# Optimization experiments

Measured on AMD Instinct MI355X. Metric: run time of the kernel, lower is better.

## Reference

```python
import jax, jax.numpy as jnp
import numpy as np

B, S, D, H, W = 4, 2048, 512, 8, 16
DK = D // H


def setup_inputs() -> dict:
    key = jax.random.key(0)
    ks = jax.random.split(key, 11)
    scale = 1.0 / np.sqrt(D)
    return {
        "query": jax.random.normal(ks[0], (B, S, D), jnp.float32),
        "key": jax.random.normal(ks[1], (B, S, D), jnp.float32),
        "value": jax.random.normal(ks[2], (B, S, D), jnp.float32),
        "Wq": jax.random.normal(ks[3], (D, D), jnp.float32) * scale,
        "bq": jnp.zeros((D,), jnp.float32),
        "Wk": jax.random.normal(ks[4], (D, D), jnp.float32) * scale,
        "bk": jnp.zeros((D,), jnp.float32),
        "Wv": jax.random.normal(ks[5], (D, D), jnp.float32) * scale,
        "bv": jnp.zeros((D,), jnp.float32),
        "Wo": jax.random.normal(ks[6], (D, D), jnp.float32) * scale,
        "bo": jnp.zeros((D,), jnp.float32),
    }


def reference(query, key, value, Wq, bq, Wk, bk, Wv, bv, Wo, bo):
    b, s, d = query.shape
    # QKV projections -> [b, H, s, DK]
    Q = (query @ Wq + bq).reshape(b, s, H, DK).transpose(0, 2, 1, 3)
    K = (key @ Wk + bk).reshape(b, s, H, DK).transpose(0, 2, 1, 3)
    V = (value @ Wv + bv).reshape(b, s, H, DK).transpose(0, 2, 1, 3)
    # Dense scores (faithful to original O(n^2) math), then static band mask
    scores = jnp.einsum("bhqd,bhkd->bhqk", Q, K) / jnp.sqrt(jnp.array(DK, scores_dtype := Q.dtype))
    idx = jnp.arange(s)
    local = jnp.abs(idx[:, None] - idx[None, :]) <= W  # [s, s] band
    mask_value = jnp.finfo(scores.dtype).min
    scores = jnp.where(local[None, None], scores, mask_value)
    attn = jax.nn.softmax(scores, axis=-1)
    ctx = jnp.einsum("bhqk,bhkd->bhqd", attn, V)
    ctx = ctx.transpose(0, 2, 1, 3).reshape(b, s, d)
    return ctx @ Wo + bo
```

## Files before the change

### kernel.cpp

```cpp
#include <hip/hip_runtime.h>

typedef __attribute__((ext_vector_type(8))) short bf16x8;
typedef __attribute__((ext_vector_type(4))) float f32x4;
typedef __attribute__((ext_vector_type(4))) unsigned int u32x4;
typedef __attribute__((ext_vector_type(8))) unsigned short bfu8;
typedef __attribute__((ext_vector_type(4))) unsigned short bfu4;

#define BB 4
#define SS 2048
#define DD 512
#define HH 8
#define DKK 64
#define WWIN 16
#define MTOT (BB*SS)
#define MKE  ((long)MTOT*DD)
#define NKE  ((long)DD*DD)

__device__ __forceinline__ unsigned short f2bf(float f) {
  unsigned int u = __float_as_uint(f);
  u += 0x7fffu + ((u >> 16) & 1u);
  return (unsigned short)(u >> 16);
}
__device__ __forceinline__ float bf2f(unsigned short s) {
  return __uint_as_float(((unsigned int)s) << 16);
}

__device__ __forceinline__ void gload_lds16(const unsigned short* g, unsigned short* l) {
  __builtin_amdgcn_global_load_lds((const __attribute__((address_space(1))) void*)g,
                                   (__attribute__((address_space(3))) void*)l, 16, 0, 0);
}

__global__ __launch_bounds__(256) void convert_w(
    const float* __restrict__ Wq, const float* __restrict__ Wk,
    const float* __restrict__ Wv, const float* __restrict__ Wo,
    const float* __restrict__ bq, const float* __restrict__ bk, const float* __restrict__ bv,
    unsigned short* __restrict__ wt, float* __restrict__ bias_all)
{
  int bx = blockIdx.x;
  if (bx >= 256) {
    int idx = (bx - 256) * 256 + threadIdx.x;
    bias_all[idx] = idx < DD ? bq[idx] : (idx < 2*DD ? bk[idx-DD] : bv[idx-2*DD]);
    return;
  }
  int wm = bx >> 6;
  int tile = bx & 63;
  int tr = tile >> 3, tc = tile & 7;
  const float* src = wm==0 ? Wq : wm==1 ? Wk : wm==2 ? Wv : Wo;
  unsigned short* dst = wt + (long)wm*NKE;
  __shared__ float tl[64][65];
  int t = threadIdx.x;
  int cr = t >> 6;
  int cc = t & 63;
  for (int p = 0; p < 16; ++p) {
    int row = p*4 + cr;
    tl[row][cc] = src[(long)(tr*64+row)*DD + tc*64 + cc];
  }
  __syncthreads();
  for (int p = 0; p < 16; ++p) {
    int orow = p*4 + cr;
    dst[(long)(tc*64 + orow)*DD + tr*64 + cc] = f2bf(tl[cc][orow]);
  }
}

template<int OUT_BF16, int A_FP32>
__global__ __launch_bounds__(256, 2) void gemm_kernel(
    const void* __restrict__ a0, const void* __restrict__ a1, const void* __restrict__ a2,
    const unsigned short* __restrict__ Btbase, long bZ,
    const float* __restrict__ biasBase, long biasZ,
    void* __restrict__ outBase, long outZ,
    int M, int N, int K)
{
  const int z = blockIdx.z;
  const void* Av = z==0 ? a0 : z==1 ? a1 : a2;
  const unsigned short* Bt = Btbase + (long)z*bZ;
  const float* bias = biasBase + (long)z*biasZ;

  const int tid  = threadIdx.x;
  const int lane = tid & 63;
  const int w    = tid >> 6;
  const int wr   = w >> 1, wc = w & 1;
  const int m0   = blockIdx.y * 128;
  const int n0   = blockIdx.x * 128;

  __shared__ unsigned short lA[128*64];
  __shared__ unsigned short lB[128*64];

  f32x4 acc[4][4] = {};

  for (int kt = 0; kt < K; kt += 64) {
    for (int i = 0; i < 4; ++i) {
      int e   = (w*4+i)*512 + lane*8;
      int row = e >> 6, col = e & 63;
      gload_lds16(Bt + (long)(n0 + row)*K + kt + col, &lB[(w*4+i)*512]);
    }
    if (A_FP32) {
      const float* Afp = (const float*)Av;
      for (int i = 0; i < 8; ++i) {
        int e   = (i*256 + tid) * 4;
        int row = e >> 6, col = e & 63;
        float4 f = *(const float4*)(Afp + (long)(m0 + row)*K + kt + col);
        bfu4 o;
        o[0]=f2bf(f.x); o[1]=f2bf(f.y); o[2]=f2bf(f.z); o[3]=f2bf(f.w);
        *(bfu4*)(&lA[e]) = o;
      }
    } else {
      const unsigned short* A = (const unsigned short*)Av;
      for (int i = 0; i < 4; ++i) {
        int e   = (w*4+i)*512 + lane*8;
        int row = e >> 6, col = e & 63;
        gload_lds16(A + (long)(m0 + row)*K + kt + col, &lA[(w*4+i)*512]);
      }
    }
    __syncthreads();
    for (int kk = 0; kk < 2; ++kk) {
      bf16x8 af[4], bfr[4];
      for (int m = 0; m < 4; ++m) {
        int row = wr*64 + m*16 + (lane & 15);
        af[m] = *reinterpret_cast<const bf16x8*>(&lA[row*64 + kk*32 + (lane>>4)*8]);
      }
      for (int n = 0; n < 4; ++n) {
        int col = wc*64 + n*16 + (lane & 15);
        bfr[n] = *reinterpret_cast<const bf16x8*>(&lB[col*64 + kk*32 + (lane>>4)*8]);
      }
      for (int m = 0; m < 4; ++m)
        for (int n = 0; n < 4; ++n)
          acc[m][n] = __builtin_amdgcn_mfma_f32_16x16x32_bf16(af[m], bfr[n], acc[m][n], 0, 0, 0);
    }
    __syncthreads();
  }

  for (int m = 0; m < 4; ++m) {
    int rbase = m0 + wr*64 + m*16 + ((lane>>4)<<2);
    for (int n = 0; n < 4; ++n) {
      int col = n0 + wc*64 + n*16 + (lane & 15);
      float bv = bias[col];
      for (int r = 0; r < 4; ++r) {
        float val = acc[m][n][r] + bv;
        long idx = (long)z*outZ + (long)(rbase + r)*N + col;
        if (OUT_BF16) ((unsigned short*)outBase)[idx] = f2bf(val);
        else          ((float*)outBase)[idx] = val;
      }
    }
  }
}

#define KP 76
#define PP 76
__global__ __launch_bounds__(256) void attn_kernel(
    const unsigned short* __restrict__ Qbf, const unsigned short* __restrict__ Kbf,
    const unsigned short* __restrict__ Vbf, unsigned short* __restrict__ ctxbf)
{
  const int q0 = blockIdx.x * 128;
  const int h  = blockIdx.y;
  const int b  = blockIdx.z;
  const int tid = threadIdx.x, lane = tid & 63, w = tid >> 6;
  const int c = lane & 15, g = lane >> 4;
  const int w0 = q0 - WWIN;

  __shared__ unsigned short K_l[160*KP];
  __shared__ unsigned short V_l[160*KP];
  __shared__ unsigned short P_l[4][32*PP];

  const long baseRow = (long)b*SS*DD + (long)h*DKK;
  const int qw0   = q0 + w*32;
  const int kbase = w*32;

  bf16x8 aq[2][2];
  for (int m = 0; m < 2; ++m)
    for (int kk = 0; kk < 2; ++kk)
      aq[m][kk] = *reinterpret_cast<const bf16x8*>(
          Qbf + baseRow + (long)(qw0 + m*16 + c)*DD + kk*32 + g*8);

  for (int i = 0; i < 5; ++i) {
    int u = i*256 + tid;
    int row = u >> 3, c8 = (u & 7) * 8;
    int gk = w0 + row;
    u32x4 kv = {0,0,0,0}, vv = {0,0,0,0};
    if (gk >= 0 && gk < SS) {
      kv = *(const u32x4*)(Kbf + baseRow + (long)gk*DD + c8);
      vv = *(const u32x4*)(Vbf + baseRow + (long)gk*DD + c8);
    }
    *(u32x4*)(&K_l[row*KP + c8]) = kv;
    *(u32x4*)(&V_l[row*KP + c8]) = vv;
  }
  __syncthreads();

  f32x4 accs[2][4] = {};
  __builtin_amdgcn_s_setprio(1);
  for (int kk = 0; kk < 2; ++kk) {
    bf16x8 bk[4];
    for (int n = 0; n < 4; ++n)
      bk[n] = *reinterpret_cast<const bf16x8*>(&K_l[(kbase + n*16 + c)*KP + kk*32 + g*8]);
    for (int m = 0; m < 2; ++m)
      for (int n = 0; n < 4; ++n)
        accs[m][n] = __builtin_amdgcn_mfma_f32_16x16x32_bf16(aq[m][kk], bk[n], accs[m][n], 0, 0, 0);
  }
  __builtin_amdgcn_s_setprio(0);

  float pden[2][4];
  for (int m = 0; m < 2; ++m) {
    for (int r = 0; r < 4; ++r) {
      int qi = m*16 + g*4 + r;
      float sv[4];
      float mx = -INFINITY;
      for (int n = 0; n < 4; ++n) {
        int kr = n*16 + c;
        int d  = kr - qi;
        int kg = w0 + kbase + kr;
        bool ok = (d >= 0) && (d <= 2*WWIN) && (kg >= 0) && (kg < SS);
        sv[n] = ok ? accs[m][n][r] * 0.125f : -INFINITY;
        mx = fmaxf(mx, sv[n]);
      }
      for (int off = 1; off < 16; off <<= 1) mx = fmaxf(mx, __shfl_xor(mx, off, 64));
      float sum = 0.f;
      for (int n = 0; n < 4; ++n) {
        float e = __expf(sv[n] - mx);
        sum += e;
        P_l[w][(m*16 + g*4 + r)*PP + n*16 + c] = f2bf(e);
      }
      for (int off = 1; off < 16; off <<= 1) sum += __shfl_xor(sum, off, 64);
      pden[m][r] = sum;
    }
  }
  __syncthreads();

  f32x4 acco[2][4] = {};
  for (int kk = 0; kk < 2; ++kk) {
    bf16x8 pa[2];
    for (int m = 0; m < 2; ++m)
      pa[m] = *reinterpret_cast<const bf16x8*>(&P_l[w][(m*16 + c)*PP + kk*32 + g*8]);
    bf16x8 bv[4];
    int kb = kbase + kk*32 + g*8;
    for (int n = 0; n < 4; ++n) {
      bfu8 t;
      for (int j = 0; j < 8; ++j) t[j] = V_l[(kb + j)*KP + n*16 + c];
      bv[n] = *reinterpret_cast<bf16x8*>(&t);
    }
    __builtin_amdgcn_s_setprio(1);
    for (int m = 0; m < 2; ++m)
      for (int n = 0; n < 4; ++n)
        acco[m][n] = __builtin_amdgcn_mfma_f32_16x16x32_bf16(pa[m], bv[n], acco[m][n], 0, 0, 0);
    __builtin_amdgcn_s_setprio(0);
  }

  for (int m = 0; m < 2; ++m) {
    for (int r = 0; r < 4; ++r) {
      int q = qw0 + m*16 + g*4 + r;
      float inv = 1.f / pden[m][r];
      for (int n = 0; n < 4; ++n)
        ctxbf[baseRow + (long)q*DD + n*16 + c] = f2bf(acco[m][n][r] * inv);
    }
  }
}

extern "C" void kernel_launch(void* const* d_in, const int* in_sizes, int n_in,
                              void* d_out, int out_size, void* d_ws, size_t ws_size,
                              hipStream_t stream) {
  const float* q  = (const float*)d_in[0];
  const float* k  = (const float*)d_in[1];
  const float* v  = (const float*)d_in[2];
  const float* Wq = (const float*)d_in[3];
  const float* bq = (const float*)d_in[4];
  const float* Wk = (const float*)d_in[5];
  const float* bk = (const float*)d_in[6];
  const float* Wv = (const float*)d_in[7];
  const float* bv = (const float*)d_in[8];
  const float* Wo = (const float*)d_in[9];
  const float* bo = (const float*)d_in[10];

  char* ws = (char*)d_ws;
  unsigned short* wtbf     = (unsigned short*)(ws);
  float*          bias_all = (float*)(ws + 2097152);
  unsigned short* qkvbf    = (unsigned short*)(ws + 2103296);
  unsigned short* ctxbf    = (unsigned short*)(ws + 27269120);

  convert_w<<<262, 256, 0, stream>>>(Wq, Wk, Wv, Wo, bq, bk, bv, wtbf, bias_all);
  gemm_kernel<1,1><<<dim3(4, 64, 3), 256, 0, stream>>>(
      q, k, v, wtbf, NKE, bias_all, DD,
      (void*)qkvbf, MKE, MTOT, DD, DD);
  attn_kernel<<<dim3(SS/128, HH, BB), 256, 0, stream>>>(
      qkvbf, qkvbf + MKE, qkvbf + 2*MKE, ctxbf);
  gemm_kernel<0,0><<<dim3(4, 64, 1), 256, 0, stream>>>(
      ctxbf, ctxbf, ctxbf, wtbf + 3*NKE, 0, bo, 0,
      (void*)d_out, 0, MTOT, DD, DD);
}
```

Baseline: 160.8 us.

## Replace 128x128 GEMM tiles with 32-row panels spanning the full output width

The projection GEMMs now give each block 32 rows of A and all 512 output columns, instead of a 128x128 tile. Each A row, including the fp32 inputs converted to bf16, is loaded and converted only once rather than once per column tile. Each wave computes a 32x128 slice as 2x8 MFMA tiles. The cost is that every block streams the whole 512x64 weight slab into a 64KB LDS buffer per k-step. That raises total L2 traffic for the weights and the LDS footprint per block, which may limit occupancy.

```diff
diff --git a/kernel.cpp b/kernel.cpp
--- a/kernel.cpp
+++ b/kernel.cpp
@@ -4,7 +4,6 @@
 typedef __attribute__((ext_vector_type(4))) float f32x4;
 typedef __attribute__((ext_vector_type(4))) unsigned int u32x4;
 typedef __attribute__((ext_vector_type(8))) unsigned short bfu8;
-typedef __attribute__((ext_vector_type(4))) unsigned short bfu4;
 
 #define BB 4
 #define SS 2048
@@ -63,76 +62,67 @@
 }
 
 template<int OUT_BF16, int A_FP32>
-__global__ __launch_bounds__(256, 2) void gemm_kernel(
+__global__ __launch_bounds__(256, 2) void gemm_rowpanel(
     const void* __restrict__ a0, const void* __restrict__ a1, const void* __restrict__ a2,
     const unsigned short* __restrict__ Btbase, long bZ,
     const float* __restrict__ biasBase, long biasZ,
     void* __restrict__ outBase, long outZ,
-    int M, int N, int K)
+    int N, int K)
 {
   const int z = blockIdx.z;
   const void* Av = z==0 ? a0 : z==1 ? a1 : a2;
   const unsigned short* Bt = Btbase + (long)z*bZ;
   const float* bias = biasBase + (long)z*biasZ;
 
-  const int tid  = threadIdx.x;
-  const int lane = tid & 63;
-  const int w    = tid >> 6;
-  const int wr   = w >> 1, wc = w & 1;
-  const int m0   = blockIdx.y * 128;
-  const int n0   = blockIdx.x * 128;
-
-  __shared__ unsigned short lA[128*64];
-  __shared__ unsigned short lB[128*64];
-
-  f32x4 acc[4][4] = {};
+  const int tid = threadIdx.x, lane = tid & 63, w = tid >> 6;
+  const int c = lane & 15, g = lane >> 4;
+  const int m0 = blockIdx.x * 32;
+
+  __shared__ unsigned short lA[32*64];
+  __shared__ unsigned short lB[512*64];
+
+  f32x4 acc[2][8] = {};
 
   for (int kt = 0; kt < K; kt += 64) {
-    for (int i = 0; i < 4; ++i) {
-      int e   = (w*4+i)*512 + lane*8;
-      int row = e >> 6, col = e & 63;
-      gload_lds16(Bt + (long)(n0 + row)*K + kt + col, &lB[(w*4+i)*512]);
-    }
-    if (A_FP32) {
-      const float* Afp = (const float*)Av;
-      for (int i = 0; i < 8; ++i) {
-        int e   = (i*256 + tid) * 4;
-        int row = e >> 6, col = e & 63;
-        float4 f = *(const float4*)(Afp + (long)(m0 + row)*K + kt + col);
-        bfu4 o;
-        o[0]=f2bf(f.x); o[1]=f2bf(f.y); o[2]=f2bf(f.z); o[3]=f2bf(f.w);
-        *(bfu4*)(&lA[e]) = o;
-      }
-    } else {
-      const unsigned short* A = (const unsigned short*)Av;
-      for (int i = 0; i < 4; ++i) {
-        int e   = (w*4+i)*512 + lane*8;
-        int row = e >> 6, col = e & 63;
-        gload_lds16(A + (long)(m0 + row)*K + kt + col, &lA[(w*4+i)*512]);
+    for (int i = 0; i < 16; ++i) {
+      int u = i*256 + tid;
+      int row = u >> 3, col = (u & 7) * 8;
+      gload_lds16(Bt + (long)row*K + kt + col, &lB[i*2048 + w*512]);
+    }
+    {
+      int row = tid >> 3, col = (tid & 7) * 8;
+      if (A_FP32) {
+        const float* Afp = (const float*)Av;
+        const float* src = Afp + (long)(m0 + row)*K + kt + col;
+        float4 f0 = *(const float4*)src;
+        float4 f1 = *(const float4*)(src + 4);
+        bfu8 o;
+        o[0]=f2bf(f0.x); o[1]=f2bf(f0.y); o[2]=f2bf(f0.z); o[3]=f2bf(f0.w);
+        o[4]=f2bf(f1.x); o[5]=f2bf(f1.y); o[6]=f2bf(f1.z); o[7]=f2bf(f1.w);
+        *(bfu8*)&lA[tid*8] = o;
+      } else {
+        const unsigned short* A = (const unsigned short*)Av;
+        gload_lds16(A + (long)(m0 + row)*K + kt + col, &lA[w*512]);
       }
     }
     __syncthreads();
     for (int kk = 0; kk < 2; ++kk) {
-      bf16x8 af[4], bfr[4];
-      for (int m = 0; m < 4; ++m) {
-        int row = wr*64 + m*16 + (lane & 15);
-        af[m] = *reinterpret_cast<const bf16x8*>(&lA[row*64 + kk*32 + (lane>>4)*8]);
-      }
-      for (int n = 0; n < 4; ++n) {
-        int col = wc*64 + n*16 + (lane & 15);
-        bfr[n] = *reinterpret_cast<const bf16x8*>(&lB[col*64 + kk*32 + (lane>>4)*8]);
-      }
-      for (int m = 0; m < 4; ++m)
-        for (int n = 0; n < 4; ++n)
+      bf16x8 af[2], bfr[8];
+      for (int m = 0; m < 2; ++m)
+        af[m] = *reinterpret_cast<const bf16x8*>(&lA[(m*16 + c)*64 + kk*32 + g*8]);
+      for (int n = 0; n < 8; ++n)
+        bfr[n] = *reinterpret_cast<const bf16x8*>(&lB[(w*128 + n*16 + c)*64 + kk*32 + g*8]);
+      for (int m = 0; m < 2; ++m)
+        for (int n = 0; n < 8; ++n)
           acc[m][n] = __builtin_amdgcn_mfma_f32_16x16x32_bf16(af[m], bfr[n], acc[m][n], 0, 0, 0);
     }
     __syncthreads();
   }
 
-  for (int m = 0; m < 4; ++m) {
-    int rbase = m0 + wr*64 + m*16 + ((lane>>4)<<2);
-    for (int n = 0; n < 4; ++n) {
-      int col = n0 + wc*64 + n*16 + (lane & 15);
+  for (int m = 0; m < 2; ++m) {
+    int rbase = m0 + m*16 + g*4;
+    for (int n = 0; n < 8; ++n) {
+      int col = w*128 + n*16 + c;
       float bv = bias[col];
       for (int r = 0; r < 4; ++r) {
         float val = acc[m][n][r] + bv;
@@ -275,12 +265,12 @@
   unsigned short* ctxbf    = (unsigned short*)(ws + 27269120);
 
   convert_w<<<262, 256, 0, stream>>>(Wq, Wk, Wv, Wo, bq, bk, bv, wtbf, bias_all);
-  gemm_kernel<1,1><<<dim3(4, 64, 3), 256, 0, stream>>>(
+  gemm_rowpanel<1,1><<<dim3(MTOT/32, 1, 3), 256, 0, stream>>>(
       q, k, v, wtbf, NKE, bias_all, DD,
-      (void*)qkvbf, MKE, MTOT, DD, DD);
+      (void*)qkvbf, MKE, DD, DD);
   attn_kernel<<<dim3(SS/128, HH, BB), 256, 0, stream>>>(
       qkvbf, qkvbf + MKE, qkvbf + 2*MKE, ctxbf);
-  gemm_kernel<0,0><<<dim3(4, 64, 1), 256, 0, stream>>>(
+  gemm_rowpanel<0,0><<<dim3(MTOT/32, 1, 1), 256, 0, stream>>>(
       ctxbf, ctxbf, ctxbf, wtbf + 3*NKE, 0, bo, 0,
-      (void*)d_out, 0, MTOT, DD, DD);
-}
+      (void*)d_out, 0, DD, DD);
+}
```

New measurement: 168.8 us. 5.0% more time.
